# Performance work log

Measured on AMD Instinct MI355X. Metric: run time of the kernel, lower is better.

Reference implementation:

```python
import jax, jax.numpy as jnp
import numpy as np

B, L = 16, 2048          # batch, raw history length
H, S, M = 512, 8, 512    # hidden_dim, sequence_count, max_seq_len
V = 32000                # shared embed_tokens vocab
TG = 64                  # TIME_GAP_BUCKET_COUNT
LN_EPS = 1e-5


def setup_inputs() -> dict:
    key = jax.random.key(0)
    ks = jax.random.split(key, 16)
    f = lambda k, shp, scale=0.02: jax.random.normal(k, shp, jnp.float32) * scale
    return {
        "history_tokens": jax.random.randint(ks[0], (B, L), 0, V),
        "history_post_tokens": jax.random.randint(ks[1], (B, L), 0, V),
        "history_author_tokens": jax.random.randint(ks[2], (B, L), 0, V),
        "history_action_tokens": jax.random.randint(ks[3], (B, L), 0, V),
        "history_time_gap": jax.random.randint(ks[4], (B, L), 0, TG + 1),
        "history_group_ids": jax.random.randint(ks[5], (B, L), 0, S + 1),
        "history_mask": jax.random.randint(ks[6], (B, L), 0, 2).astype(bool),
        "embed_table": f(ks[7], (V, H)),
        "time_gap_table": f(ks[8], (TG + 1, H)).at[0].set(0.0),   # padding_idx=0
        "seq_id_table": f(ks[9], (S + 1, H)).at[0].set(0.0),      # padding_idx=0
        "pos_table": f(ks[10], (M, H)),
        "ln_gamma": jnp.ones((5 * H,), jnp.float32),
        "ln_beta": jnp.zeros((5 * H,), jnp.float32),
        "w1": f(ks[11], (5 * H, 4 * H)),
        "b1": jnp.zeros((4 * H,), jnp.float32),
        "w2": f(ks[12], (4 * H, H)),
        "b2": jnp.zeros((H,), jnp.float32),
        "empty_tokens": f(ks[13], (S, H)),
    }


def _forward(embed_table, time_gap_table, seq_id_table, pos_table, ln_gamma, ln_beta,
             w1, b1, w2, b2, empty_tokens,
             history_tokens, history_post_tokens, history_author_tokens,
             history_action_tokens, history_time_gap, history_group_ids, history_mask):
    # --- event feature construction: 4 shared-vocab lookups + time-gap embedding ---
    h = embed_table[history_tokens]            # [B,L,H]
    p = embed_table[history_post_tokens]
    a = embed_table[history_author_tokens]
    act = embed_table[history_action_tokens]
    gap_idx = jnp.clip(history_time_gap, 0, TG)
    gap = time_gap_table[gap_idx] * (gap_idx != 0)[..., None]  # padding_idx=0 -> zero vec
    x = jnp.concatenate([h, p, a, act, gap], axis=-1)           # [B,L,5H]

    # --- event_projection: LayerNorm -> Linear -> SiLU -> (Dropout eval) -> Linear ---
    mu = x.mean(-1, keepdims=True)
    var = x.var(-1, keepdims=True)
    xn = (x - mu) * jax.lax.rsqrt(var + LN_EPS) * ln_gamma + ln_beta
    mid = jax.nn.silu(xn @ w1 + b1)                             # [B,L,4H]
    event = mid @ w2 + b2                                       # [B,L,H]

    # --- ragged regroup: for each (b, s) gather masked positions with group id s+1,
    #     keep the LAST M of them, scatter to slots 0..count-1 ---
    gid = history_group_ids                                     # [B,L]
    match = history_mask[:, None, :] & (gid[:, None, :] == jnp.arange(1, S + 1)[None, :, None])  # [B,S,L]
    cum = jnp.cumsum(match.astype(jnp.int32), axis=-1)          # rank+1 within group
    count = cum[..., -1]                                        # [B,S]
    offset = jnp.maximum(count - M, 0)                          # drop all but last M
    slot = cum - 1 - offset[..., None]                          # [B,S,L]
    keep = match & (slot >= 0)
    slot = jnp.where(keep, slot, M)                             # M is out-of-range -> dropped

    b_idx = jnp.arange(B)[:, None, None]
    s_idx = jnp.arange(S)[None, :, None]
    states = jnp.zeros((B, S, M, H), event.dtype)
    states = states.at[b_idx, s_idx, slot].set(event[:, None, :, :], mode="drop")
    smask = jnp.zeros((B, S, M), bool)
    smask = smask.at[b_idx, s_idx, slot].set(True, mode="drop")

    # empty groups get the learned empty token at slot 0
    empty = count == 0                                          # [B,S]
    states = states.at[:, :, 0, :].set(
        jnp.where(empty[..., None], empty_tokens[None], states[:, :, 0, :]))
    smask = smask.at[:, :, 0].set(smask[:, :, 0] | empty)

    # positional + sequence-id embeddings, then zero padded slots
    pos = pos_table[None, None]                                 # [1,1,M,H]
    sid = seq_id_table[1:S + 1][None, :, None, :]               # [1,S,1,H]
    states = (states + pos + sid) * smask[..., None].astype(states.dtype)
    return states, smask


def reference(history_tokens, history_post_tokens, history_author_tokens,
              history_action_tokens, history_time_gap, history_group_ids, history_mask,
              embed_table, time_gap_table, seq_id_table, pos_table, ln_gamma, ln_beta,
              w1, b1, w2, b2, empty_tokens):
    return _forward(embed_table, time_gap_table, seq_id_table, pos_table, ln_gamma, ln_beta,
                    w1, b1, w2, b2, empty_tokens,
                    history_tokens, history_post_tokens, history_author_tokens,
                    history_action_tokens, history_time_gap, history_group_ids, history_mask)
```

## Files before the change

kernel.cpp:

```cpp
#include <hip/hip_runtime.h>
#include <hip/hip_bf16.h>
#include <stdint.h>

#define B_ 16
#define L_ 2048
#define H_ 512
#define S_ 8
#define M_ 512
#define TG_ 64
#define NTOK (B_ * L_)
#define FIVEH (5 * H_)
#define FOURH (4 * H_)

typedef __attribute__((ext_vector_type(4))) float f32x4;
typedef __attribute__((ext_vector_type(8))) short bf16x8;

__device__ __forceinline__ short f2bf(float f) {
  unsigned u = __builtin_bit_cast(unsigned, f);
  unsigned r = (u + 0x7FFFu + ((u >> 16) & 1u)) >> 16;
  return (short)r;
}

__device__ __forceinline__ void gload_lds16(const void* g, void* l) {
  __builtin_amdgcn_global_load_lds(
      (const __attribute__((address_space(1))) unsigned int*)g,
      (__attribute__((address_space(3))) unsigned int*)l, 16, 0, 0);
}

#define BAR __builtin_amdgcn_s_barrier()
#define LGKM0 do { asm volatile("s_waitcnt lgkmcnt(0)" ::: "memory"); \
                   __builtin_amdgcn_sched_barrier(0); } while (0)
#define VMW(n) asm volatile("s_waitcnt vmcnt(" #n ")" ::: "memory")
#define PRIO(p) __builtin_amdgcn_s_setprio(p)


#define STAGE(src, isB, slot, half, kt) do {                                  \
    const short* _s = (src) + (size_t)((half) * 128) * K + (kt);              \
    const int _o = ((isB) ? 65536 : 0) + (slot) * 32768 + (half) * 16384;     \
    gload_lds16(_s + (size_t)sr0 * K + sc0, lds + _o + db0);                  \
    gload_lds16(_s + (size_t)sr1 * K + sc1, lds + _o + db1);                  \
  } while (0)

#define LDA(qr, slot) do { const int _b = (slot) * 32768 + aW + (qr) * 8192;  \
    _Pragma("unroll") for (int fm = 0; fm < 4; ++fm)                          \
    _Pragma("unroll") for (int ks = 0; ks < 2; ++ks)                          \
      a[fm][ks] = *(const bf16x8*)(lds + _b + sA[fm][ks]); } while (0)

#define LDB(dst, qc, slot) do { const int _b = (slot) * 32768 + bW + (qc) * 4096; \
    _Pragma("unroll") for (int fn = 0; fn < 2; ++fn)                          \
    _Pragma("unroll") for (int ks = 0; ks < 2; ++ks)                          \
      dst[fn][ks] = *(const bf16x8*)(lds + _b + sB[fn][ks]); } while (0)

#define MFMA16(qr, qc, bs) do {                                               \
    _Pragma("unroll") for (int fm = 0; fm < 4; ++fm)                          \
    _Pragma("unroll") for (int fn = 0; fn < 2; ++fn)                          \
    _Pragma("unroll") for (int ks = 0; ks < 2; ++ks)                          \
      acc[(qr)*4+fm][(qc)*2+fn] = __builtin_amdgcn_mfma_f32_16x16x32_bf16(    \
          a[fm][ks], bs[fn][ks], acc[(qr)*4+fm][(qc)*2+fn], 0, 0, 0); } while (0)

template<int K>
__device__ __forceinline__ void gemm_core(const short* __restrict__ Ag,
                                          const short* __restrict__ Bg,
                                          char* lds, f32x4 (&acc)[8][4],
                                          int tid) {
  constexpr int NITER = K / 128;
  const int lane = tid & 63;
  const int wave = tid >> 6;
  const int wm = wave >> 2;
  const int wn = wave & 3;
  const int la = lane & 15;
  const int hi = lane >> 4;

  const int x = (la & 7) << 4;
  int sA[4][2], sB[2][2];
#pragma unroll
  for (int fm = 0; fm < 4; ++fm)
#pragma unroll
    for (int ks = 0; ks < 2; ++ks)
      sA[fm][ks] = (((fm * 16 + la) * 128) + (ks * 32 + hi * 8) * 2) ^ x;
#pragma unroll
  for (int fn = 0; fn < 2; ++fn)
#pragma unroll
    for (int ks = 0; ks < 2; ++ks)
      sB[fn][ks] = ((((wn & 1) * 64 + fn * 16 + la) * 128) + (ks * 32 + hi * 8) * 2) ^ x;
  const int aW = wm * 16384;
  const int bW = 65536 + (wn >> 1) * 16384;

  const int db0 = tid * 16, db1 = tid * 16 + 8192;
  const int lb0 = db0 ^ (((db0 >> 7) & 7) << 4);
  const int lb1 = db1 ^ (((db1 >> 7) & 7) << 4);
  const int sr0 = lb0 >> 7, sc0 = (lb0 & 127) >> 1;
  const int sr1 = lb1 >> 7, sc1 = (lb1 & 127) >> 1;

  bf16x8 a[4][2], b0v[2][2], b1v[2][2];

  STAGE(Bg, 1, 0, 0, 0); STAGE(Bg, 1, 0, 1, 0);
  STAGE(Ag, 0, 0, 0, 0); STAGE(Ag, 0, 0, 1, 0);
  STAGE(Bg, 1, 1, 0, 64); STAGE(Bg, 1, 1, 1, 64);
  VMW(0);
  BAR;

  for (int i = 0; i < NITER - 1; ++i) {
    const int kt1 = (2 * i + 1) * 64, kt2 = kt1 + 64, kt3 = kt1 + 128;
    LDA(0, 0); LDB(b0v, 0, 0); STAGE(Ag, 0, 1, 0, kt1);
    BAR; LGKM0; PRIO(1); MFMA16(0, 0, b0v); PRIO(0); BAR;
    LDB(b1v, 1, 0); STAGE(Ag, 0, 1, 1, kt1);
    BAR; LGKM0; PRIO(1); MFMA16(0, 1, b1v); PRIO(0); BAR;
    LDA(1, 0); STAGE(Bg, 1, 0, 0, kt2);
    BAR; LGKM0; PRIO(1); MFMA16(1, 1, b1v); PRIO(0); BAR;
    STAGE(Bg, 1, 0, 1, kt2);
    BAR; LGKM0; PRIO(1); MFMA16(1, 0, b0v); PRIO(0); VMW(4); BAR;
    LDA(0, 1); LDB(b0v, 0, 1); STAGE(Ag, 0, 0, 0, kt2);
    BAR; LGKM0; PRIO(1); MFMA16(0, 0, b0v); PRIO(0); BAR;
    LDB(b1v, 1, 1); STAGE(Ag, 0, 0, 1, kt2);
    BAR; LGKM0; PRIO(1); MFMA16(0, 1, b1v); PRIO(0); BAR;
    LDA(1, 1); STAGE(Bg, 1, 1, 0, kt3);
    BAR; LGKM0; PRIO(1); MFMA16(1, 1, b1v); PRIO(0); BAR;
    STAGE(Bg, 1, 1, 1, kt3);
    BAR; LGKM0; PRIO(1); MFMA16(1, 0, b0v); PRIO(0); VMW(4); BAR;
  }
  {
    const int kt1 = (2 * (NITER - 1) + 1) * 64;
    LDA(0, 0); LDB(b0v, 0, 0); STAGE(Ag, 0, 1, 0, kt1);
    BAR; LGKM0; PRIO(1); MFMA16(0, 0, b0v); PRIO(0); BAR;
    LDB(b1v, 1, 0); STAGE(Ag, 0, 1, 1, kt1);
    BAR; LGKM0; PRIO(1); MFMA16(0, 1, b1v); PRIO(0); BAR;
    LDA(1, 0);
    BAR; LGKM0; PRIO(1); MFMA16(1, 1, b1v); PRIO(0); BAR;
    BAR; LGKM0; PRIO(1); MFMA16(1, 0, b0v); PRIO(0); VMW(0); BAR;
    LDA(0, 1); LDB(b0v, 0, 1);
    BAR; LGKM0; PRIO(1); MFMA16(0, 0, b0v); PRIO(0); BAR;
    LDB(b1v, 1, 1);
    BAR; LGKM0; PRIO(1); MFMA16(0, 1, b1v); PRIO(0); BAR;
    LDA(1, 1);
    BAR; LGKM0; PRIO(1); MFMA16(1, 1, b1v); PRIO(0); BAR;
    BAR; LGKM0; PRIO(1); MFMA16(1, 0, b0v); PRIO(0);
  }
}

__global__ __launch_bounds__(512, 2) void gemm1_kernel(
    const short* __restrict__ A, const short* __restrict__ Bt,
    const float* __restrict__ bias, const int* __restrict__ nkeep,
    short* __restrict__ C) {
  const int nbm = (nkeep[0] + 255) >> 8;
  const int local = blockIdx.x >> 3;
  if (local >= nbm) return;
  const int T = (blockIdx.x & 7) * nbm + local;
  const int bm = T >> 3, bn = T & 7;
  __shared__ __align__(16) char lds[131072];
  const int tid = threadIdx.x;
  f32x4 acc[8][4] = {};
  gemm_core<FIVEH>(A + (size_t)bm * 256 * FIVEH, Bt + (size_t)bn * 256 * FIVEH,
                   lds, acc, tid);
  const int lane = tid & 63, wave = tid >> 6;
  const int wm = wave >> 2, wn = wave & 3;
  const int la = lane & 15, hi = lane >> 4;
  const int row0 = bm * 256 + wm * 128 + hi * 4;
  const int col0 = bn * 256 + wn * 64 + la;
#pragma unroll
  for (int mi = 0; mi < 8; ++mi)
#pragma unroll
    for (int ni = 0; ni < 4; ++ni) {
      const int col = col0 + ni * 16;
      const float bv = bias[col];
#pragma unroll
      for (int r = 0; r < 4; ++r) {
        const int row = row0 + mi * 16 + r;
        float v = acc[mi][ni][r] + bv;
        float sg = 1.f / (1.f + __expf(-v));
        C[(size_t)row * FOURH + col] = f2bf(v * sg);
      }
    }
}

#define ASL(s) ((s) * 32768)
#define BSL(s) (98304 + (s) * 16384)

#define STG2(src, ldsoff, kt) do {                                            \
    const short* _s = (src) + (kt);                                          \
    gload_lds16(_s + (size_t)sr0 * 2048 + sc0, lds + (ldsoff) + db0);         \
    gload_lds16(_s + (size_t)sr1 * 2048 + sc1, lds + (ldsoff) + db1);         \
  } while (0)

#define LDA2(slot) do { const int _b = ASL(slot) + aW2;                       \
    _Pragma("unroll") for (int fm = 0; fm < 4; ++fm)                          \
    _Pragma("unroll") for (int ks = 0; ks < 2; ++ks)                          \
      a[fm][ks] = *(const bf16x8*)(lds + _b + sA2[fm][ks]); } while (0)

#define LDB2a(slot) do { const int _b = BSL(slot);                            \
    _Pragma("unroll") for (int fn = 0; fn < 2; ++fn)                          \
    _Pragma("unroll") for (int ks = 0; ks < 2; ++ks)                          \
      b[fn][ks] = *(const bf16x8*)(lds + _b + sB2[fn][ks]); } while (0)

#define LDB2b(slot) do { const int _b = BSL(slot);                            \
    _Pragma("unroll") for (int fn = 2; fn < 4; ++fn)                          \
    _Pragma("unroll") for (int ks = 0; ks < 2; ++ks)                          \
      b[fn][ks] = *(const bf16x8*)(lds + _b + sB2[fn][ks]); } while (0)

#define MFMA2(h) do {                                                         \
    _Pragma("unroll") for (int fm = 0; fm < 4; ++fm)                          \
    _Pragma("unroll") for (int fn = 2*(h); fn < 2*(h)+2; ++fn)                \
    _Pragma("unroll") for (int ks = 0; ks < 2; ++ks)                          \
      acc[fm][fn] = __builtin_amdgcn_mfma_f32_16x16x32_bf16(                  \
          a[fm][ks], b[fn][ks], acc[fm][fn], 0, 0, 0); } while (0)

#define T2(slot, kt, ISSUE, WAITC) do {                                       \
    LDA2(slot); LDB2a(slot);                                                  \
    if (ISSUE) STG2(Ag, ASL(((slot) + 2) % 3), kt);                           \
    BAR; LGKM0; PRIO(1); MFMA2(0); PRIO(0); BAR;                              \
    LDB2b(slot);                                                              \
    if (ISSUE) { STG2(Ag + 128 * 2048, ASL(((slot) + 2) % 3) + 16384, kt);    \
                 STG2(Bg, BSL(((slot) + 2) % 3), kt); }                       \
    BAR; LGKM0; PRIO(1); MFMA2(1); PRIO(0); WAITC; BAR;                       \
  } while (0)

__global__ __launch_bounds__(512) void gemm2_kernel(
    const short* __restrict__ A, const short* __restrict__ Bt,
    const float* __restrict__ b2, const float* __restrict__ pos,
    const float* __restrict__ sidtab, const int* __restrict__ destv,
    const int* __restrict__ nkeep, float* __restrict__ states) {
  const int bn = blockIdx.x & 3;
  const int bm = blockIdx.x >> 2;
  const int nk = nkeep[0];
  if (bm * 256 >= nk) return;
  __shared__ __align__(16) char lds[147456];
  const int tid = threadIdx.x;
  const int lane = tid & 63, wave = tid >> 6;
  const int wm = wave >> 1;
  const int wn = wave & 1;
  const int la = lane & 15, hi = lane >> 4;
  const short* Ag = A + (size_t)bm * 256 * 2048;
  const short* Bg = Bt + (size_t)bn * 128 * 2048;

  const int x = (la & 7) << 4;
  int sA2[4][2], sB2[4][2];
#pragma unroll
  for (int fm = 0; fm < 4; ++fm)
#pragma unroll
    for (int ks = 0; ks < 2; ++ks)
      sA2[fm][ks] = ((((wm & 1) * 64 + fm * 16 + la) * 128) + (ks * 32 + hi * 8) * 2) ^ x;
#pragma unroll
  for (int fn = 0; fn < 4; ++fn)
#pragma unroll
    for (int ks = 0; ks < 2; ++ks)
      sB2[fn][ks] = (((wn * 64 + fn * 16 + la) * 128) + (ks * 32 + hi * 8) * 2) ^ x;
  const int aW2 = (wm >> 1) * 16384;

  const int db0 = tid * 16, db1 = tid * 16 + 8192;
  const int lb0 = db0 ^ (((db0 >> 7) & 7) << 4);
  const int lb1 = db1 ^ (((db1 >> 7) & 7) << 4);
  const int sr0 = lb0 >> 7, sc0 = (lb0 & 127) >> 1;
  const int sr1 = lb1 >> 7, sc1 = (lb1 & 127) >> 1;

  f32x4 acc[4][4] = {};
  bf16x8 a[4][2], b[4][2];

  STG2(Ag, ASL(0), 0); STG2(Ag + 128 * 2048, ASL(0) + 16384, 0); STG2(Bg, BSL(0), 0);
  STG2(Ag, ASL(1), 64); STG2(Ag + 128 * 2048, ASL(1) + 16384, 64); STG2(Bg, BSL(1), 64);
  VMW(6);
  BAR;
  for (int i = 0; i < 10; ++i) {
    const int kt = i * 192 + 128;
    T2(0, kt, true, VMW(6));
    T2(1, kt + 64, true, VMW(6));
    T2(2, kt + 128, true, VMW(6));
  }
  T2(0, 0, false, VMW(0));
  T2(1, 0, false, ((void)0));

  const int row0 = bm * 256 + wm * 64 + hi * 4;
  const int col0 = bn * 128 + wn * 64 + la;
#pragma unroll
  for (int mi = 0; mi < 4; ++mi) {
#pragma unroll
    for (int r = 0; r < 4; ++r) {
      const int row = row0 + mi * 16 + r;
      if (row >= nk) continue;
      const int dest = destv[row];
      const int slot = dest & (M_ - 1);
      const int gs = dest >> 9;
      const int s = gs & (S_ - 1);
      float* orow = states + (size_t)dest * H_;
#pragma unroll
      for (int n = 0; n < 4; ++n) {
        const int col = col0 + n * 16;
        orow[col] = acc[mi][n][r] + b2[col] + pos[slot * H_ + col] +
                    sidtab[(s + 1) * H_ + col];
      }
    }
  }
}

__global__ __launch_bounds__(256) void transpose_cvt_kernel(
    const float* __restrict__ w1, short* __restrict__ w1T,
    const float* __restrict__ w2, short* __restrict__ w2T) {
  const float* in;
  short* out;
  int K, N;
  if (blockIdx.z == 0) { in = w1; out = w1T; K = FIVEH; N = FOURH; }
  else                 { in = w2; out = w2T; K = FOURH; N = H_; }
  const int n0 = blockIdx.x * 32, k0 = blockIdx.y * 32;
  if (n0 >= N || k0 >= K) return;
  __shared__ float tile[32][33];
  const int tx = threadIdx.x, ty = threadIdx.y;
#pragma unroll
  for (int i = 0; i < 32; i += 8)
    tile[ty + i][tx] = in[(size_t)(k0 + ty + i) * N + n0 + tx];
  __syncthreads();
#pragma unroll
  for (int i = 0; i < 32; i += 8)
    out[(size_t)(n0 + ty + i) * K + k0 + tx] = f2bf(tile[tx][ty + i]);
}

__global__ __launch_bounds__(256) void scan_kernel(
    const int* __restrict__ gid, const int* __restrict__ mask,
    int* __restrict__ counts, int* __restrict__ tokidx,
    int* __restrict__ destv, int* __restrict__ nkeep) {
  const int b = blockIdx.x >> 3;
  const int s = blockIdx.x & 7;
  const int g = s + 1;
  const int base = b * L_;
  const int t = threadIdx.x;
  int loc = 0, sum = 0;
  const int l0 = t * 8;
#pragma unroll
  for (int j = 0; j < 8; ++j) {
    int l = l0 + j;
    bool mt = (mask[base + l] != 0) && (gid[base + l] == g);
    loc |= (mt ? 1 : 0) << j;
    sum += mt ? 1 : 0;
  }
  __shared__ int lds[256];
  __shared__ int basep, offs;
  lds[t] = sum;
  __syncthreads();
  for (int off = 1; off < 256; off <<= 1) {
    int vv = (t >= off) ? lds[t - off] : 0;
    __syncthreads();
    lds[t] += vv;
    __syncthreads();
  }
  if (t == 255) {
    const int cnt = lds[255];
    counts[blockIdx.x] = cnt;
    const int kc = cnt < M_ ? cnt : M_;
    offs = cnt - kc;
    basep = atomicAdd(nkeep, kc);
  }
  __syncthreads();
  int run = lds[t] - sum;
  const int gsM = blockIdx.x * M_;
#pragma unroll
  for (int j = 0; j < 8; ++j) {
    if ((loc >> j) & 1) {
      run += 1;
      const int slot = run - 1 - offs;
      if (slot >= 0) {
        tokidx[basep + slot] = base + l0 + j;
        destv[basep + slot] = gsM + slot;
      }
    }
  }
}

__global__ __launch_bounds__(256) void gather_ln_kernel(
    const int* __restrict__ tokidx, const int* __restrict__ nkeep,
    const int* __restrict__ tok0, const int* __restrict__ tok1,
    const int* __restrict__ tok2, const int* __restrict__ tok3,
    const int* __restrict__ tgap,
    const float* __restrict__ emb, const float* __restrict__ gaptab,
    const float* __restrict__ gamma, const float* __restrict__ beta,
    short* __restrict__ xn) {
  const int wid = threadIdx.x >> 6;
  const int l = threadIdx.x & 63;
  const int j = blockIdx.x * 4 + wid;
  const int nk = nkeep[0];
  const int padded = (nk + 255) & ~255;
  if (j >= padded) return;
  short* orow = xn + (size_t)j * FIVEH;
  if (j >= nk) {
    short4 z = make_short4(0, 0, 0, 0);
#pragma unroll
    for (int i = 0; i < 10; ++i) ((short4*)orow)[i * 64 + l] = z;
    return;
  }
  const int token = tokidx[j];
  const int tk0 = tok0[token], tk1 = tok1[token], tk2 = tok2[token],
            tk3 = tok3[token];
  int gi = tgap[token];
  gi = gi < 0 ? 0 : (gi > TG_ ? TG_ : gi);
  const float4* sb[5];
  sb[0] = (const float4*)(emb + (size_t)tk0 * H_);
  sb[1] = (const float4*)(emb + (size_t)tk1 * H_);
  sb[2] = (const float4*)(emb + (size_t)tk2 * H_);
  sb[3] = (const float4*)(emb + (size_t)tk3 * H_);
  sb[4] = (const float4*)(gaptab + (size_t)gi * H_);
  float4 v[10];
  float sum = 0.f, sq = 0.f;
#pragma unroll
  for (int i = 0; i < 10; ++i) {
    const int d4 = i * 64 + l;
    const int seg = i >> 1;
    float4 xv;
    if (seg < 4 || gi != 0) xv = sb[seg][d4 & 127];
    else xv = make_float4(0.f, 0.f, 0.f, 0.f);
    v[i] = xv;
    sum += xv.x + xv.y + xv.z + xv.w;
    sq += xv.x * xv.x + xv.y * xv.y + xv.z * xv.z + xv.w * xv.w;
  }
#pragma unroll
  for (int s = 32; s; s >>= 1) {
    sum += __shfl_xor(sum, s, 64);
    sq += __shfl_xor(sq, s, 64);
  }
  const float mu = sum * (1.f / FIVEH);
  const float var = sq * (1.f / FIVEH) - mu * mu;
  const float rs = rsqrtf(var + 1e-5f);
#pragma unroll
  for (int i = 0; i < 10; ++i) {
    const int d4 = i * 64 + l;
    const float4 g4 = ((const float4*)gamma)[d4];
    const float4 b4 = ((const float4*)beta)[d4];
    short4 o;
    o.x = f2bf((v[i].x - mu) * rs * g4.x + b4.x);
    o.y = f2bf((v[i].y - mu) * rs * g4.y + b4.y);
    o.z = f2bf((v[i].z - mu) * rs * g4.z + b4.z);
    o.w = f2bf((v[i].w - mu) * rs * g4.w + b4.w);
    ((short4*)orow)[d4] = o;
  }
}

__global__ __launch_bounds__(256) void finalize_kernel(
    const int* __restrict__ counts, const float* __restrict__ empty_tok,
    const float* __restrict__ pos, const float* __restrict__ sidtab,
    float* __restrict__ states, float* __restrict__ smask) {
  const int total = B_ * S_ * M_ * (H_ / 4);
  for (int idx = blockIdx.x * 256 + threadIdx.x; idx < total;
       idx += gridDim.x * 256) {
    const int row = idx >> 7, c = idx & 127;
    const int gs = row >> 9, m = row & (M_ - 1), s = gs & (S_ - 1);
    const int cnt = counts[gs];
    const bool empty = (cnt == 0);
    const bool filled = m < (cnt < M_ ? cnt : M_);
    if (c == 0) smask[row] = (filled || (empty && m == 0)) ? 1.0f : 0.0f;
    if (filled) continue;
    float4 o = make_float4(0.f, 0.f, 0.f, 0.f);
    if (empty && m == 0) {
      float4 e = ((const float4*)(empty_tok + s * H_))[c];
      float4 pv = ((const float4*)pos)[c];
      float4 sd = ((const float4*)(sidtab + (s + 1) * H_))[c];
      o.x = e.x + pv.x + sd.x;
      o.y = e.y + pv.y + sd.y;
      o.z = e.z + pv.z + sd.z;
      o.w = e.w + pv.w + sd.w;
    }
    ((float4*)(states + (size_t)row * H_))[c] = o;
  }
}

extern "C" void kernel_launch(void* const* d_in, const int* in_sizes, int n_in,
                              void* d_out, int out_size, void* d_ws, size_t ws_size,
                              hipStream_t stream) {
  const int* tok0 = (const int*)d_in[0];
  const int* tok1 = (const int*)d_in[1];
  const int* tok2 = (const int*)d_in[2];
  const int* tok3 = (const int*)d_in[3];
  const int* tgap = (const int*)d_in[4];
  const int* gid = (const int*)d_in[5];
  const int* mask = (const int*)d_in[6];
  const float* emb = (const float*)d_in[7];
  const float* gaptab = (const float*)d_in[8];
  const float* sidtab = (const float*)d_in[9];
  const float* pos = (const float*)d_in[10];
  const float* gamma = (const float*)d_in[11];
  const float* beta = (const float*)d_in[12];
  const float* w1 = (const float*)d_in[13];
  const float* b1 = (const float*)d_in[14];
  const float* w2 = (const float*)d_in[15];
  const float* b2 = (const float*)d_in[16];
  const float* empty_tok = (const float*)d_in[17];

  char* p = (char*)d_ws;
  short* xn = (short*)p;  p += (size_t)NTOK * FIVEH * 2;
  short* mid = (short*)p; p += (size_t)NTOK * FOURH * 2;
  short* w1T = (short*)p; p += (size_t)FOURH * FIVEH * 2;
  short* w2T = (short*)p; p += (size_t)H_ * FOURH * 2;
  int* tokidx = (int*)p;  p += (size_t)NTOK * 4;
  int* destv = (int*)p;   p += (size_t)NTOK * 4;
  int* counts = (int*)p;  p += 512;
  int* nkeep = (int*)p;   p += 512;

  float* states = (float*)d_out;
  float* smask = states + (size_t)B_ * S_ * M_ * H_;

  hipMemsetAsync(nkeep, 0, 4, stream);
  transpose_cvt_kernel<<<dim3(FOURH / 32, FIVEH / 32, 2), dim3(32, 8), 0, stream>>>(
      w1, w1T, w2, w2T);
  scan_kernel<<<B_ * S_, 256, 0, stream>>>(gid, mask, counts, tokidx, destv,
                                           nkeep);
  gather_ln_kernel<<<NTOK / 4, 256, 0, stream>>>(tokidx, nkeep, tok0, tok1, tok2,
                                                 tok3, tgap, emb, gaptab, gamma,
                                                 beta, xn);
  gemm1_kernel<<<128 * 8, 512, 0, stream>>>(xn, w1T, b1, nkeep, mid);
  gemm2_kernel<<<128 * 4, 512, 0, stream>>>(mid, w2T, b2, pos, sidtab, destv,
                                            nkeep, states);
  finalize_kernel<<<2048, 256, 0, stream>>>(counts, empty_tok, pos, sidtab,
                                            states, smask);
}
```

Measured before the change: 264.6 us.

## Triple-buffer A in gemm1, merge prep kernels, fuse finalize into gemm2

Gemm1 now keeps three rotating LDS slots for A tiles and two for B, prefetching A two k-steps ahead. LDS grows to 160KB, so occupancy drops from two blocks per CU to one. The weight transpose and the group scan are merged into one prep kernel. The finalize pass becomes extra blocks of the gemm2 launch, which removes two kernel launches and lets the padding fill overlap the GEMM. The risk is that the lost gemm1 occupancy costs more than the deeper prefetch gains.

```diff
diff --git a/kernel.cpp b/kernel.cpp
--- a/kernel.cpp
+++ b/kernel.cpp
@@ -33,24 +33,6 @@
 #define VMW(n) asm volatile("s_waitcnt vmcnt(" #n ")" ::: "memory")
 #define PRIO(p) __builtin_amdgcn_s_setprio(p)
 
-
-#define STAGE(src, isB, slot, half, kt) do {                                  \
-    const short* _s = (src) + (size_t)((half) * 128) * K + (kt);              \
-    const int _o = ((isB) ? 65536 : 0) + (slot) * 32768 + (half) * 16384;     \
-    gload_lds16(_s + (size_t)sr0 * K + sc0, lds + _o + db0);                  \
-    gload_lds16(_s + (size_t)sr1 * K + sc1, lds + _o + db1);                  \
-  } while (0)
-
-#define LDA(qr, slot) do { const int _b = (slot) * 32768 + aW + (qr) * 8192;  \
-    _Pragma("unroll") for (int fm = 0; fm < 4; ++fm)                          \
-    _Pragma("unroll") for (int ks = 0; ks < 2; ++ks)                          \
-      a[fm][ks] = *(const bf16x8*)(lds + _b + sA[fm][ks]); } while (0)
-
-#define LDB(dst, qc, slot) do { const int _b = (slot) * 32768 + bW + (qc) * 4096; \
-    _Pragma("unroll") for (int fn = 0; fn < 2; ++fn)                          \
-    _Pragma("unroll") for (int ks = 0; ks < 2; ++ks)                          \
-      dst[fn][ks] = *(const bf16x8*)(lds + _b + sB[fn][ks]); } while (0)
-
 #define MFMA16(qr, qc, bs) do {                                               \
     _Pragma("unroll") for (int fm = 0; fm < 4; ++fm)                          \
     _Pragma("unroll") for (int fn = 0; fn < 2; ++fn)                          \
@@ -58,12 +40,40 @@
       acc[(qr)*4+fm][(qc)*2+fn] = __builtin_amdgcn_mfma_f32_16x16x32_bf16(    \
           a[fm][ks], bs[fn][ks], acc[(qr)*4+fm][(qc)*2+fn], 0, 0, 0); } while (0)
 
+
+#define SGA(slot, half, kt) do {                                              \
+    const short* _s = Ag + (size_t)((half) * 128 + sr0) * K + (kt) + sc0;     \
+    const short* _t = Ag + (size_t)((half) * 128 + sr1) * K + (kt) + sc1;     \
+    const int _o = (slot) * 32768 + (half) * 16384;                           \
+    gload_lds16(_s, lds + _o + db0);                                          \
+    gload_lds16(_t, lds + _o + db1);                                          \
+  } while (0)
+
+#define SGB(slot, half, kt) do {                                              \
+    const short* _s = Bg + (size_t)((half) * 128 + sr0) * K + (kt) + sc0;     \
+    const short* _t = Bg + (size_t)((half) * 128 + sr1) * K + (kt) + sc1;     \
+    const int _o = 98304 + (slot) * 32768 + (half) * 16384;                   \
+    gload_lds16(_s, lds + _o + db0);                                          \
+    gload_lds16(_t, lds + _o + db1);                                          \
+  } while (0)
+
+#define LDA1(qr, slot) do { const int _b = (slot) * 32768 + aW + (qr) * 8192; \
+    _Pragma("unroll") for (int fm = 0; fm < 4; ++fm)                          \
+    _Pragma("unroll") for (int ks = 0; ks < 2; ++ks)                          \
+      a[fm][ks] = *(const bf16x8*)(lds + _b + sA[fm][ks]); } while (0)
+
+#define LDB1(dst, qc, slot) do {                                              \
+    const int _b = 98304 + (slot) * 32768 + bW + (qc) * 4096;                 \
+    _Pragma("unroll") for (int fn = 0; fn < 2; ++fn)                          \
+    _Pragma("unroll") for (int ks = 0; ks < 2; ++ks)                          \
+      dst[fn][ks] = *(const bf16x8*)(lds + _b + sB[fn][ks]); } while (0)
+
 template<int K>
-__device__ __forceinline__ void gemm_core(const short* __restrict__ Ag,
-                                          const short* __restrict__ Bg,
-                                          char* lds, f32x4 (&acc)[8][4],
-                                          int tid) {
-  constexpr int NITER = K / 128;
+__device__ __forceinline__ void gemm1_core(const short* __restrict__ Ag,
+                                           const short* __restrict__ Bg,
+                                           char* lds, f32x4 (&acc)[8][4],
+                                           int tid) {
+  constexpr int NT = K / 64;
   const int lane = tid & 63;
   const int wave = tid >> 6;
   const int wm = wave >> 2;
@@ -84,7 +94,7 @@
     for (int ks = 0; ks < 2; ++ks)
       sB[fn][ks] = ((((wn & 1) * 64 + fn * 16 + la) * 128) + (ks * 32 + hi * 8) * 2) ^ x;
   const int aW = wm * 16384;
-  const int bW = 65536 + (wn >> 1) * 16384;
+  const int bW = (wn >> 1) * 16384;
 
   const int db0 = tid * 16, db1 = tid * 16 + 8192;
   const int lb0 = db0 ^ (((db0 >> 7) & 7) << 4);
@@ -94,51 +104,53 @@
 
   bf16x8 a[4][2], b0v[2][2], b1v[2][2];
 
-  STAGE(Bg, 1, 0, 0, 0); STAGE(Bg, 1, 0, 1, 0);
-  STAGE(Ag, 0, 0, 0, 0); STAGE(Ag, 0, 0, 1, 0);
-  STAGE(Bg, 1, 1, 0, 64); STAGE(Bg, 1, 1, 1, 64);
-  VMW(0);
+  SGA(0, 0, 0); SGA(0, 1, 0);
+  SGB(0, 0, 0); SGB(0, 1, 0);
+  SGA(1, 0, 64); SGA(1, 1, 64);
+  VMW(4);
   BAR;
 
-  for (int i = 0; i < NITER - 1; ++i) {
-    const int kt1 = (2 * i + 1) * 64, kt2 = kt1 + 64, kt3 = kt1 + 128;
-    LDA(0, 0); LDB(b0v, 0, 0); STAGE(Ag, 0, 1, 0, kt1);
+  int as = 0, bs = 0;
+  for (int t = 0; t < NT - 2; ++t) {
+    const int as2 = (as >= 1) ? as - 1 : as + 2;
+    const int bs1 = bs ^ 1;
+    const int ktB = (t + 1) * 64, ktA = (t + 2) * 64;
+    LDA1(0, as); LDB1(b0v, 0, bs); SGB(bs1, 0, ktB);
     BAR; LGKM0; PRIO(1); MFMA16(0, 0, b0v); PRIO(0); BAR;
-    LDB(b1v, 1, 0); STAGE(Ag, 0, 1, 1, kt1);
+    LDB1(b1v, 1, bs); SGB(bs1, 1, ktB);
     BAR; LGKM0; PRIO(1); MFMA16(0, 1, b1v); PRIO(0); BAR;
-    LDA(1, 0); STAGE(Bg, 1, 0, 0, kt2);
+    LDA1(1, as); SGA(as2, 0, ktA);
     BAR; LGKM0; PRIO(1); MFMA16(1, 1, b1v); PRIO(0); BAR;
-    STAGE(Bg, 1, 0, 1, kt2);
+    SGA(as2, 1, ktA);
     BAR; LGKM0; PRIO(1); MFMA16(1, 0, b0v); PRIO(0); VMW(4); BAR;
-    LDA(0, 1); LDB(b0v, 0, 1); STAGE(Ag, 0, 0, 0, kt2);
+    as = (as >= 2) ? 0 : as + 1;
+    bs = bs1;
+  }
+  {
+    const int bs1 = bs ^ 1;
+    const int ktB = (NT - 1) * 64;
+    LDA1(0, as); LDB1(b0v, 0, bs); SGB(bs1, 0, ktB);
     BAR; LGKM0; PRIO(1); MFMA16(0, 0, b0v); PRIO(0); BAR;
-    LDB(b1v, 1, 1); STAGE(Ag, 0, 0, 1, kt2);
+    LDB1(b1v, 1, bs); SGB(bs1, 1, ktB);
     BAR; LGKM0; PRIO(1); MFMA16(0, 1, b1v); PRIO(0); BAR;
-    LDA(1, 1); STAGE(Bg, 1, 1, 0, kt3);
-    BAR; LGKM0; PRIO(1); MFMA16(1, 1, b1v); PRIO(0); BAR;
-    STAGE(Bg, 1, 1, 1, kt3);
-    BAR; LGKM0; PRIO(1); MFMA16(1, 0, b0v); PRIO(0); VMW(4); BAR;
-  }
-  {
-    const int kt1 = (2 * (NITER - 1) + 1) * 64;
-    LDA(0, 0); LDB(b0v, 0, 0); STAGE(Ag, 0, 1, 0, kt1);
-    BAR; LGKM0; PRIO(1); MFMA16(0, 0, b0v); PRIO(0); BAR;
-    LDB(b1v, 1, 0); STAGE(Ag, 0, 1, 1, kt1);
-    BAR; LGKM0; PRIO(1); MFMA16(0, 1, b1v); PRIO(0); BAR;
-    LDA(1, 0);
+    LDA1(1, as);
     BAR; LGKM0; PRIO(1); MFMA16(1, 1, b1v); PRIO(0); BAR;
     BAR; LGKM0; PRIO(1); MFMA16(1, 0, b0v); PRIO(0); VMW(0); BAR;
-    LDA(0, 1); LDB(b0v, 0, 1);
+    as = (as >= 2) ? 0 : as + 1;
+    bs = bs1;
+  }
+  {
+    LDA1(0, as); LDB1(b0v, 0, bs);
     BAR; LGKM0; PRIO(1); MFMA16(0, 0, b0v); PRIO(0); BAR;
-    LDB(b1v, 1, 1);
+    LDB1(b1v, 1, bs);
     BAR; LGKM0; PRIO(1); MFMA16(0, 1, b1v); PRIO(0); BAR;
-    LDA(1, 1);
+    LDA1(1, as);
     BAR; LGKM0; PRIO(1); MFMA16(1, 1, b1v); PRIO(0); BAR;
     BAR; LGKM0; PRIO(1); MFMA16(1, 0, b0v); PRIO(0);
   }
 }
 
-__global__ __launch_bounds__(512, 2) void gemm1_kernel(
+__global__ __launch_bounds__(512, 1) void gemm1_kernel(
     const short* __restrict__ A, const short* __restrict__ Bt,
     const float* __restrict__ bias, const int* __restrict__ nkeep,
     short* __restrict__ C) {
@@ -147,11 +159,11 @@
   if (local >= nbm) return;
   const int T = (blockIdx.x & 7) * nbm + local;
   const int bm = T >> 3, bn = T & 7;
-  __shared__ __align__(16) char lds[131072];
+  __shared__ __align__(16) char lds[163840];
   const int tid = threadIdx.x;
   f32x4 acc[8][4] = {};
-  gemm_core<FIVEH>(A + (size_t)bm * 256 * FIVEH, Bt + (size_t)bn * 256 * FIVEH,
-                   lds, acc, tid);
+  gemm1_core<FIVEH>(A + (size_t)bm * 256 * FIVEH, Bt + (size_t)bn * 256 * FIVEH,
+                    lds, acc, tid);
   const int lane = tid & 63, wave = tid >> 6;
   const int wm = wave >> 2, wn = wave & 3;
   const int la = lane & 15, hi = lane >> 4;
@@ -214,11 +226,38 @@
     BAR; LGKM0; PRIO(1); MFMA2(1); PRIO(0); WAITC; BAR;                       \
   } while (0)
 
-__global__ __launch_bounds__(512) void gemm2_kernel(
+__global__ __launch_bounds__(512) void gemm2fin_kernel(
     const short* __restrict__ A, const short* __restrict__ Bt,
     const float* __restrict__ b2, const float* __restrict__ pos,
     const float* __restrict__ sidtab, const int* __restrict__ destv,
-    const int* __restrict__ nkeep, float* __restrict__ states) {
+    const int* __restrict__ nkeep, const int* __restrict__ counts,
+    const float* __restrict__ empty_tok, float* __restrict__ states,
+    float* __restrict__ smask) {
+  if (blockIdx.x >= 512) {
+    const int total = B_ * S_ * M_ * (H_ / 4);
+    for (int idx = (blockIdx.x - 512) * 512 + threadIdx.x; idx < total;
+         idx += 512 * 512) {
+      const int row = idx >> 7, c = idx & 127;
+      const int gs = row >> 9, m = row & (M_ - 1), s = gs & (S_ - 1);
+      const int cnt = counts[gs];
+      const bool empty = (cnt == 0);
+      const bool filled = m < (cnt < M_ ? cnt : M_);
+      if (c == 0) smask[row] = (filled || (empty && m == 0)) ? 1.0f : 0.0f;
+      if (filled) continue;
+      float4 o = make_float4(0.f, 0.f, 0.f, 0.f);
+      if (empty && m == 0) {
+        float4 e = ((const float4*)(empty_tok + s * H_))[c];
+        float4 pv = ((const float4*)pos)[c];
+        float4 sd = ((const float4*)(sidtab + (s + 1) * H_))[c];
+        o.x = e.x + pv.x + sd.x;
+        o.y = e.y + pv.y + sd.y;
+        o.z = e.z + pv.z + sd.z;
+        o.w = e.w + pv.w + sd.w;
+      }
+      ((float4*)(states + (size_t)row * H_))[c] = o;
+    }
+    return;
+  }
   const int bn = blockIdx.x & 3;
   const int bm = blockIdx.x >> 2;
   const int nk = nkeep[0];
@@ -291,33 +330,35 @@
   }
 }
 
-__global__ __launch_bounds__(256) void transpose_cvt_kernel(
+__global__ __launch_bounds__(256) void prep_kernel(
     const float* __restrict__ w1, short* __restrict__ w1T,
-    const float* __restrict__ w2, short* __restrict__ w2T) {
-  const float* in;
-  short* out;
-  int K, N;
-  if (blockIdx.z == 0) { in = w1; out = w1T; K = FIVEH; N = FOURH; }
-  else                 { in = w2; out = w2T; K = FOURH; N = H_; }
-  const int n0 = blockIdx.x * 32, k0 = blockIdx.y * 32;
-  if (n0 >= N || k0 >= K) return;
-  __shared__ float tile[32][33];
-  const int tx = threadIdx.x, ty = threadIdx.y;
-#pragma unroll
-  for (int i = 0; i < 32; i += 8)
-    tile[ty + i][tx] = in[(size_t)(k0 + ty + i) * N + n0 + tx];
-  __syncthreads();
-#pragma unroll
-  for (int i = 0; i < 32; i += 8)
-    out[(size_t)(n0 + ty + i) * K + k0 + tx] = f2bf(tile[tx][ty + i]);
-}
-
-__global__ __launch_bounds__(256) void scan_kernel(
+    const float* __restrict__ w2, short* __restrict__ w2T,
     const int* __restrict__ gid, const int* __restrict__ mask,
     int* __restrict__ counts, int* __restrict__ tokidx,
     int* __restrict__ destv, int* __restrict__ nkeep) {
-  const int b = blockIdx.x >> 3;
-  const int s = blockIdx.x & 7;
+  const int bid = blockIdx.x;
+  if (bid < 6144) {
+    const float* in;
+    short* out;
+    int K, N, tt;
+    if (bid < 5120) { in = w1; out = w1T; K = FIVEH; N = FOURH; tt = bid; }
+    else            { in = w2; out = w2T; K = FOURH; N = H_;   tt = bid - 5120; }
+    const int nT = N >> 5;
+    const int n0 = (tt % nT) * 32, k0 = (tt / nT) * 32;
+    __shared__ float tile[32][33];
+    const int tx = threadIdx.x & 31, ty = threadIdx.x >> 5;
+#pragma unroll
+    for (int i = 0; i < 32; i += 8)
+      tile[ty + i][tx] = in[(size_t)(k0 + ty + i) * N + n0 + tx];
+    __syncthreads();
+#pragma unroll
+    for (int i = 0; i < 32; i += 8)
+      out[(size_t)(n0 + ty + i) * K + k0 + tx] = f2bf(tile[tx][ty + i]);
+    return;
+  }
+  const int grp = bid - 6144;
+  const int b = grp >> 3;
+  const int s = grp & 7;
   const int g = s + 1;
   const int base = b * L_;
   const int t = threadIdx.x;
@@ -330,26 +371,26 @@
     loc |= (mt ? 1 : 0) << j;
     sum += mt ? 1 : 0;
   }
-  __shared__ int lds[256];
+  __shared__ int sdata[256];
   __shared__ int basep, offs;
-  lds[t] = sum;
+  sdata[t] = sum;
   __syncthreads();
   for (int off = 1; off < 256; off <<= 1) {
-    int vv = (t >= off) ? lds[t - off] : 0;
+    int vv = (t >= off) ? sdata[t - off] : 0;
     __syncthreads();
-    lds[t] += vv;
+    sdata[t] += vv;
     __syncthreads();
   }
   if (t == 255) {
-    const int cnt = lds[255];
-    counts[blockIdx.x] = cnt;
+    const int cnt = sdata[255];
+    counts[grp] = cnt;
     const int kc = cnt < M_ ? cnt : M_;
     offs = cnt - kc;
     basep = atomicAdd(nkeep, kc);
   }
   __syncthreads();
-  int run = lds[t] - sum;
-  const int gsM = blockIdx.x * M_;
+  int run = sdata[t] - sum;
+  const int gsM = grp * M_;
 #pragma unroll
   for (int j = 0; j < 8; ++j) {
     if ((loc >> j) & 1) {
@@ -427,34 +468,6 @@
     o.z = f2bf((v[i].z - mu) * rs * g4.z + b4.z);
     o.w = f2bf((v[i].w - mu) * rs * g4.w + b4.w);
     ((short4*)orow)[d4] = o;
-  }
-}
-
-__global__ __launch_bounds__(256) void finalize_kernel(
-    const int* __restrict__ counts, const float* __restrict__ empty_tok,
-    const float* __restrict__ pos, const float* __restrict__ sidtab,
-    float* __restrict__ states, float* __restrict__ smask) {
-  const int total = B_ * S_ * M_ * (H_ / 4);
-  for (int idx = blockIdx.x * 256 + threadIdx.x; idx < total;
-       idx += gridDim.x * 256) {
-    const int row = idx >> 7, c = idx & 127;
-    const int gs = row >> 9, m = row & (M_ - 1), s = gs & (S_ - 1);
-    const int cnt = counts[gs];
-    const bool empty = (cnt == 0);
-    const bool filled = m < (cnt < M_ ? cnt : M_);
-    if (c == 0) smask[row] = (filled || (empty && m == 0)) ? 1.0f : 0.0f;
-    if (filled) continue;
-    float4 o = make_float4(0.f, 0.f, 0.f, 0.f);
-    if (empty && m == 0) {
-      float4 e = ((const float4*)(empty_tok + s * H_))[c];
-      float4 pv = ((const float4*)pos)[c];
-      float4 sd = ((const float4*)(sidtab + (s + 1) * H_))[c];
-      o.x = e.x + pv.x + sd.x;
-      o.y = e.y + pv.y + sd.y;
-      o.z = e.z + pv.z + sd.z;
-      o.w = e.w + pv.w + sd.w;
-    }
-    ((float4*)(states + (size_t)row * H_))[c] = o;
   }
 }
 
@@ -494,16 +507,13 @@
   float* smask = states + (size_t)B_ * S_ * M_ * H_;
 
   hipMemsetAsync(nkeep, 0, 4, stream);
-  transpose_cvt_kernel<<<dim3(FOURH / 32, FIVEH / 32, 2), dim3(32, 8), 0, stream>>>(
-      w1, w1T, w2, w2T);
-  scan_kernel<<<B_ * S_, 256, 0, stream>>>(gid, mask, counts, tokidx, destv,
-                                           nkeep);
+  prep_kernel<<<6272, 256, 0, stream>>>(w1, w1T, w2, w2T, gid, mask, counts,
+                                        tokidx, destv, nkeep);
   gather_ln_kernel<<<NTOK / 4, 256, 0, stream>>>(tokidx, nkeep, tok0, tok1, tok2,
                                                  tok3, tgap, emb, gaptab, gamma,
                                                  beta, xn);
   gemm1_kernel<<<128 * 8, 512, 0, stream>>>(xn, w1T, b1, nkeep, mid);
-  gemm2_kernel<<<128 * 4, 512, 0, stream>>>(mid, w2T, b2, pos, sidtab, destv,
-                                            nkeep, states);
-  finalize_kernel<<<2048, 256, 0, stream>>>(counts, empty_tok, pos, sidtab,
-                                            states, smask);
-}
+  gemm2fin_kernel<<<512 + 512, 512, 0, stream>>>(mid, w2T, b2, pos, sidtab,
+                                                 destv, nkeep, counts, empty_tok,
+                                                 states, smask);
+}
```

New measurement: 274.7 us. 1.04x slower.
